# Performance work log

Measured on AMD Instinct MI355X. Metric: run time of the kernel, lower is better.

Reference implementation:

```python
import jax, jax.numpy as jnp
import numpy as np

EPS = 1e-5

def binarize(x):
    # sign with 0 -> -1
    return jnp.where(x <= 0, -1.0, 1.0).astype(x.dtype)

def conv2d(x, w, stride=1, padding=0, dilation=1):
    return jax.lax.conv_general_dilated(
        x, w, (stride, stride), [(padding, padding), (padding, padding)],
        rhs_dilation=(dilation, dilation),
        dimension_numbers=('NCHW', 'OIHW', 'NCHW'))

def bin_conv(x, w, stride=1, padding=0, dilation=1):
    return conv2d(binarize(x), binarize(w), stride, padding, dilation)

def bn(x, g, b, m, v):
    inv = g / jnp.sqrt(v + EPS)          # [C]
    return x * inv[None, :, None, None] + (b - m * inv)[None, :, None, None]

def prelu(x, a):
    return jnp.where(x >= 0, x, a * x)   # a is scalar (nn.PReLU default)

def setup_inputs() -> dict:
    key = jax.random.key(0)
    ks = jax.random.split(key, 16)
    B, C, H, W = 8, 128, 128, 256
    Ci = C // 4  # proj_ratio = 4
    def bn_params(k, c):
        k1, k2, k3, k4 = jax.random.split(k, 4)
        return (jax.random.uniform(k1, (c,), jnp.float32, 0.5, 1.5),
                jax.random.normal(k2, (c,), jnp.float32) * 0.1,
                jax.random.normal(k3, (c,), jnp.float32) * 0.1,
                jax.random.uniform(k4, (c,), jnp.float32, 0.5, 1.5))
    g1, b1, m1, v1 = bn_params(ks[1], Ci)
    g2, b2, m2, v2 = bn_params(ks[3], Ci)
    g3, b3, m3, v3 = bn_params(ks[5], C)
    return {
        'x': jax.random.normal(ks[0], (B, C, H, W), jnp.float32),
        'w1': jax.random.normal(ks[6], (Ci, C, 1, 1), jnp.float32) * 0.1,
        'g1': g1, 'b1': b1, 'm1': m1, 'v1': v1,
        'a1': jnp.float32(0.25),
        'w2': jax.random.normal(ks[7], (Ci, Ci, 3, 3), jnp.float32) * 0.1,
        'g2': g2, 'b2': b2, 'm2': m2, 'v2': v2,
        'a2': jnp.float32(0.25),
        'w3': jax.random.normal(ks[8], (C, Ci, 1, 1), jnp.float32) * 0.1,
        'g3': g3, 'b3': b3, 'm3': m3, 'v3': v3,
        'a3': jnp.float32(0.25),
        'a_out': jnp.float32(0.25),
    }

def reference(x, w1, g1, b1, m1, v1, a1,
              w2, g2, b2, m2, v2, a2,
              w3, g3, b3, m3, v3, a3, a_out):
    identity = x
    h = prelu(bn(bin_conv(x, w1), g1, b1, m1, v1), a1)          # 1x1 proj
    h = prelu(bn(bin_conv(h, w2, padding=1), g2, b2, m2, v2), a2)  # 3x3
    h = prelu(bn(bin_conv(h, w3), g3, b3, m3, v3), a3)          # 1x1 expand
    return prelu(h + identity, a_out)
```

## Files before the change

### kernel.cpp

```cpp
#include <hip/hip_runtime.h>
#include <stdint.h>
#include <math.h>


#define EPS 1e-5f
constexpr int B = 8, C = 128, Ci = 32, H = 128, W = 256;
constexpr int HW = H * W;
constexpr int P  = B * HW;

constexpr int WS_S1 = 1024;
constexpr int WS_S2 = 1024 + P;

__global__ __launch_bounds__(256) void prep_kernel(
    const float* __restrict__ w1,
    const float* __restrict__ g1, const float* __restrict__ b1,
    const float* __restrict__ m1, const float* __restrict__ v1,
    const float* __restrict__ w2,
    const float* __restrict__ g2, const float* __restrict__ b2,
    const float* __restrict__ m2, const float* __restrict__ v2,
    const float* __restrict__ w3,
    const float* __restrict__ g3, const float* __restrict__ b3,
    const float* __restrict__ m3, const float* __restrict__ v3,
    uint32_t* __restrict__ ws)
{
    int t = threadIdx.x;
    float* wsf = (float*)ws;

    if (t < 128) {
        int ci = t >> 2, wd = t & 3;
        const float* src = w1 + ci * C + wd * 32;
        uint32_t m = 0;
        #pragma unroll
        for (int j = 0; j < 32; ++j) m |= (src[j] > 0.f ? 1u : 0u) << j;
        ws[t] = m;
    }
    for (int idx = t; idx < 288; idx += 256) {
        int ci = idx / 9, tap = idx % 9;
        uint32_t m = 0;
        for (int cj = 0; cj < 32; ++cj)
            m |= (w2[(ci * Ci + cj) * 9 + tap] > 0.f ? 1u : 0u) << cj;
        ws[128 + idx] = m;
    }
    if (t < 128) {
        const float* src = w3 + t * Ci;
        uint32_t m = 0;
        #pragma unroll
        for (int j = 0; j < 32; ++j) m |= (src[j] > 0.f ? 1u : 0u) << j;
        ws[416 + t] = m;
    }
    if (t < 32) {
        float inv1 = g1[t] / sqrtf(v1[t] + EPS);
        wsf[544 + t] = m1[t] - b1[t] / inv1;
        float inv2 = g2[t] / sqrtf(v2[t] + EPS);
        wsf[576 + t] = m2[t] - b2[t] / inv2;
    }
    if (t < 128) {
        float i3 = g3[t] / sqrtf(v3[t] + EPS);
        wsf[608 + t] = i3;
        wsf[736 + t] = b3[t] - m3[t] * i3;
    }
}

__global__ __launch_bounds__(256) void k1_kernel(
    const float* __restrict__ x, const uint32_t* __restrict__ ws,
    uint32_t* __restrict__ s1)
{
    __shared__ uint32_t w1p[128];
    __shared__ float T1[32];
    int t = threadIdx.x;
    if (t < 128) w1p[t] = ws[t];
    if (t < 32)  T1[t] = ((const float*)ws)[544 + t];
    __syncthreads();

    int p0  = (blockIdx.x * 256 + t) * 4;
    int b   = p0 >> 15;
    int rem = p0 & (HW - 1);
    const float4* xb = (const float4*)(x + (size_t)b * C * HW) + (rem >> 2);
    constexpr int CS = HW / 4;

    uint32_t m[4][4];
    #pragma unroll
    for (int wd = 0; wd < 4; ++wd) {
        uint32_t m0 = 0, m1 = 0, m2 = 0, m3 = 0;
        #pragma unroll
        for (int j = 0; j < 32; ++j) {
            float4 v = xb[(size_t)(wd * 32 + j) * CS];
            m0 |= (v.x > 0.f ? 1u : 0u) << j;
            m1 |= (v.y > 0.f ? 1u : 0u) << j;
            m2 |= (v.z > 0.f ? 1u : 0u) << j;
            m3 |= (v.w > 0.f ? 1u : 0u) << j;
        }
        m[0][wd] = m0; m[1][wd] = m1; m[2][wd] = m2; m[3][wd] = m3;
    }

    uint32_t o0 = 0, o1 = 0, o2 = 0, o3 = 0;
    #pragma unroll
    for (int ci = 0; ci < 32; ++ci) {
        uint32_t wa = w1p[ci * 4 + 0], wb = w1p[ci * 4 + 1];
        uint32_t wc = w1p[ci * 4 + 2], wd = w1p[ci * 4 + 3];
        float T = T1[ci];
        int n0 = __popc(m[0][0] ^ wa) + __popc(m[0][1] ^ wb) + __popc(m[0][2] ^ wc) + __popc(m[0][3] ^ wd);
        int n1 = __popc(m[1][0] ^ wa) + __popc(m[1][1] ^ wb) + __popc(m[1][2] ^ wc) + __popc(m[1][3] ^ wd);
        int n2 = __popc(m[2][0] ^ wa) + __popc(m[2][1] ^ wb) + __popc(m[2][2] ^ wc) + __popc(m[2][3] ^ wd);
        int n3 = __popc(m[3][0] ^ wa) + __popc(m[3][1] ^ wb) + __popc(m[3][2] ^ wc) + __popc(m[3][3] ^ wd);
        o0 |= ((float)(128 - 2 * n0) > T ? 1u : 0u) << ci;
        o1 |= ((float)(128 - 2 * n1) > T ? 1u : 0u) << ci;
        o2 |= ((float)(128 - 2 * n2) > T ? 1u : 0u) << ci;
        o3 |= ((float)(128 - 2 * n3) > T ? 1u : 0u) << ci;
    }
    *(uint4*)(s1 + p0) = make_uint4(o0, o1, o2, o3);
}

__global__ __launch_bounds__(256) void k2_kernel(
    const uint32_t* __restrict__ s1, const uint32_t* __restrict__ ws,
    uint32_t* __restrict__ s2)
{
    __shared__ uint32_t w2p[288];
    __shared__ float T2[32];
    int t = threadIdx.x;
    for (int i = t; i < 288; i += 256) w2p[i] = ws[128 + i];
    if (t < 32) T2[t] = ((const float*)ws)[576 + t];
    __syncthreads();

    int p   = blockIdx.x * 256 + t;
    int b   = p >> 15;
    int rem = p & (HW - 1);
    int h   = rem >> 8;
    int w   = rem & 255;

    uint32_t n[9];
    uint32_t vmask = 0;
    int nv = 0;
    #pragma unroll
    for (int dy = -1; dy <= 1; ++dy) {
        #pragma unroll
        for (int dx = -1; dx <= 1; ++dx) {
            int tap = (dy + 1) * 3 + (dx + 1);
            int hh = h + dy, wv = w + dx;
            bool ok = (hh >= 0) & (hh < H) & (wv >= 0) & (wv < W);
            uint32_t val = 0;
            if (ok) val = s1[b * HW + hh * W + wv];
            n[tap] = val;
            vmask |= ok ? (1u << tap) : 0u;
            nv += ok ? 1 : 0;
        }
    }

    uint32_t out = 0;
    #pragma unroll
    for (int ci = 0; ci < 32; ++ci) {
        int neq = 0;
        #pragma unroll
        for (int tap = 0; tap < 9; ++tap) {
            int pc = __popc(n[tap] ^ w2p[ci * 9 + tap]);
            neq += ((vmask >> tap) & 1u) ? pc : 0;
        }
        float y2 = (float)(32 * nv - 2 * neq);
        out |= (y2 > T2[ci] ? 1u : 0u) << ci;
    }
    s2[p] = out;
}

__global__ __launch_bounds__(256) void k3_kernel(
    const float* __restrict__ x, const uint32_t* __restrict__ s2,
    const uint32_t* __restrict__ ws,
    const float* __restrict__ a3p, const float* __restrict__ aoutp,
    float* __restrict__ out)
{
    __shared__ uint32_t w3p[128];
    __shared__ float inv3[128], c3[128];
    int t = threadIdx.x;
    if (t < 128) {
        w3p[t]  = ws[416 + t];
        inv3[t] = ((const float*)ws)[608 + t];
        c3[t]   = ((const float*)ws)[736 + t];
    }
    __syncthreads();

    float a3 = a3p[0], aout = aoutp[0];
    int p   = blockIdx.x * 256 + t;
    int b   = p >> 15;
    int rem = p & (HW - 1);
    size_t base = (size_t)b * C * HW + rem;
    uint32_t sw = s2[p];

    #pragma unroll 8
    for (int c = 0; c < C; ++c) {
        int y3 = 32 - 2 * __popc(sw ^ w3p[c]);
        float hv = fmaf((float)y3, inv3[c], c3[c]);
        hv = hv < 0.f ? a3 * hv : hv;
        float o = hv + x[base + (size_t)c * HW];
        o = o < 0.f ? aout * o : o;
        out[base + (size_t)c * HW] = o;
    }
}

extern "C" void kernel_launch(void* const* d_in, const int* in_sizes, int n_in,
                              void* d_out, int out_size, void* d_ws, size_t ws_size,
                              hipStream_t stream)
{
    const float* x  = (const float*)d_in[0];
    const float* w1 = (const float*)d_in[1];
    const float* g1 = (const float*)d_in[2];
    const float* b1 = (const float*)d_in[3];
    const float* m1 = (const float*)d_in[4];
    const float* v1 = (const float*)d_in[5];
    const float* w2 = (const float*)d_in[7];
    const float* g2 = (const float*)d_in[8];
    const float* b2 = (const float*)d_in[9];
    const float* m2 = (const float*)d_in[10];
    const float* v2 = (const float*)d_in[11];
    const float* w3 = (const float*)d_in[13];
    const float* g3 = (const float*)d_in[14];
    const float* b3 = (const float*)d_in[15];
    const float* m3 = (const float*)d_in[16];
    const float* v3 = (const float*)d_in[17];
    const float* a3 = (const float*)d_in[18];
    const float* ao = (const float*)d_in[19];

    uint32_t* ws = (uint32_t*)d_ws;
    uint32_t* s1 = ws + WS_S1;
    uint32_t* s2 = ws + WS_S2;
    float* out = (float*)d_out;

    hipLaunchKernelGGL(prep_kernel, dim3(1), dim3(256), 0, stream,
                       w1, g1, b1, m1, v1, w2, g2, b2, m2, v2, w3, g3, b3, m3, v3, ws);
    hipLaunchKernelGGL(k1_kernel, dim3(P / 1024), dim3(256), 0, stream, x, ws, s1);
    hipLaunchKernelGGL(k2_kernel, dim3(P / 256), dim3(256), 0, stream, s1, ws, s2);
    hipLaunchKernelGGL(k3_kernel, dim3(P / 256), dim3(256), 0, stream, x, s2, ws, a3, ao, out);
}
```

Before: 310.7 us.

## Fuse 3x3 binary conv with expand stage, four pixels per thread

Merges the 3x3 binary convolution kernel into the final expand/residual kernel so the intermediate packed bitmask never goes to global memory. Each thread now processes four adjacent pixels, reusing a 3x6 neighbourhood of loaded words across them. This removes one launch and the s2 round trip but lowers thread count and raises register pressure in the memory-bound final loop.

Result: slower. 334.5 us (+7.6%).

```diff
diff --git a/kernel.cpp b/kernel.cpp
--- a/kernel.cpp
+++ b/kernel.cpp
@@ -9,7 +9,6 @@
 constexpr int P  = B * HW;
 
 constexpr int WS_S1 = 1024;
-constexpr int WS_S2 = 1024 + P;
 
 __global__ __launch_bounds__(256) void prep_kernel(
     const float* __restrict__ w1,
@@ -111,65 +110,19 @@
     *(uint4*)(s1 + p0) = make_uint4(o0, o1, o2, o3);
 }
 
-__global__ __launch_bounds__(256) void k2_kernel(
-    const uint32_t* __restrict__ s1, const uint32_t* __restrict__ ws,
-    uint32_t* __restrict__ s2)
+__global__ __launch_bounds__(256) void k23_kernel(
+    const float* __restrict__ x, const uint32_t* __restrict__ s1,
+    const uint32_t* __restrict__ ws,
+    const float* __restrict__ a3p, const float* __restrict__ aoutp,
+    float* __restrict__ out)
 {
     __shared__ uint32_t w2p[288];
     __shared__ float T2[32];
+    __shared__ uint32_t w3p[128];
+    __shared__ float inv3[128], c3[128];
     int t = threadIdx.x;
     for (int i = t; i < 288; i += 256) w2p[i] = ws[128 + i];
     if (t < 32) T2[t] = ((const float*)ws)[576 + t];
-    __syncthreads();
-
-    int p   = blockIdx.x * 256 + t;
-    int b   = p >> 15;
-    int rem = p & (HW - 1);
-    int h   = rem >> 8;
-    int w   = rem & 255;
-
-    uint32_t n[9];
-    uint32_t vmask = 0;
-    int nv = 0;
-    #pragma unroll
-    for (int dy = -1; dy <= 1; ++dy) {
-        #pragma unroll
-        for (int dx = -1; dx <= 1; ++dx) {
-            int tap = (dy + 1) * 3 + (dx + 1);
-            int hh = h + dy, wv = w + dx;
-            bool ok = (hh >= 0) & (hh < H) & (wv >= 0) & (wv < W);
-            uint32_t val = 0;
-            if (ok) val = s1[b * HW + hh * W + wv];
-            n[tap] = val;
-            vmask |= ok ? (1u << tap) : 0u;
-            nv += ok ? 1 : 0;
-        }
-    }
-
-    uint32_t out = 0;
-    #pragma unroll
-    for (int ci = 0; ci < 32; ++ci) {
-        int neq = 0;
-        #pragma unroll
-        for (int tap = 0; tap < 9; ++tap) {
-            int pc = __popc(n[tap] ^ w2p[ci * 9 + tap]);
-            neq += ((vmask >> tap) & 1u) ? pc : 0;
-        }
-        float y2 = (float)(32 * nv - 2 * neq);
-        out |= (y2 > T2[ci] ? 1u : 0u) << ci;
-    }
-    s2[p] = out;
-}
-
-__global__ __launch_bounds__(256) void k3_kernel(
-    const float* __restrict__ x, const uint32_t* __restrict__ s2,
-    const uint32_t* __restrict__ ws,
-    const float* __restrict__ a3p, const float* __restrict__ aoutp,
-    float* __restrict__ out)
-{
-    __shared__ uint32_t w3p[128];
-    __shared__ float inv3[128], c3[128];
-    int t = threadIdx.x;
     if (t < 128) {
         w3p[t]  = ws[416 + t];
         inv3[t] = ((const float*)ws)[608 + t];
@@ -177,21 +130,92 @@
     }
     __syncthreads();
 
+    int p0  = (blockIdx.x * 256 + t) * 4;
+    int b   = p0 >> 15;
+    int rem = p0 & (HW - 1);
+    int h   = rem >> 8;
+    int w0  = rem & 255;
+
+    const uint32_t* sb = s1 + b * HW;
+    uint32_t rowv[3][6];
+    uint32_t rokm = 0, colok = 0;
+    #pragma unroll
+    for (int i = 0; i < 6; ++i) {
+        int col = w0 - 1 + i;
+        if (col >= 0 && col < W) colok |= 1u << i;
+    }
+    #pragma unroll
+    for (int r = 0; r < 3; ++r) {
+        int hh = h - 1 + r;
+        bool rok = (hh >= 0) && (hh < H);
+        if (rok) rokm |= 1u << r;
+        #pragma unroll
+        for (int i = 0; i < 6; ++i) {
+            int col = w0 - 1 + i;
+            bool ok = rok && ((colok >> i) & 1u);
+            uint32_t val = 0;
+            if (ok) val = sb[hh * W + col];
+            rowv[r][i] = val;
+        }
+    }
+
+    uint32_t vm[4]; int nv[4];
+    #pragma unroll
+    for (int k = 0; k < 4; ++k) {
+        uint32_t v = 0;
+        #pragma unroll
+        for (int r = 0; r < 3; ++r) {
+            #pragma unroll
+            for (int dx = 0; dx < 3; ++dx) {
+                bool ok = ((rokm >> r) & 1u) && ((colok >> (k + dx)) & 1u);
+                v |= ok ? (1u << (r * 3 + dx)) : 0u;
+            }
+        }
+        vm[k] = v;
+        nv[k] = __popc(v);
+    }
+
+    uint32_t s2w[4] = {0, 0, 0, 0};
+    #pragma unroll
+    for (int ci = 0; ci < 32; ++ci) {
+        uint32_t wt[9];
+        #pragma unroll
+        for (int tap = 0; tap < 9; ++tap) wt[tap] = w2p[ci * 9 + tap];
+        float T = T2[ci];
+        #pragma unroll
+        for (int k = 0; k < 4; ++k) {
+            int neq = 0;
+            #pragma unroll
+            for (int r = 0; r < 3; ++r) {
+                #pragma unroll
+                for (int dx = 0; dx < 3; ++dx) {
+                    int tap = r * 3 + dx;
+                    int pc = __popc(rowv[r][k + dx] ^ wt[tap]);
+                    neq += ((vm[k] >> tap) & 1u) ? pc : 0;
+                }
+            }
+            float y2 = (float)(32 * nv[k] - 2 * neq);
+            s2w[k] |= (y2 > T ? 1u : 0u) << ci;
+        }
+    }
+
     float a3 = a3p[0], aout = aoutp[0];
-    int p   = blockIdx.x * 256 + t;
-    int b   = p >> 15;
-    int rem = p & (HW - 1);
     size_t base = (size_t)b * C * HW + rem;
-    uint32_t sw = s2[p];
-
-    #pragma unroll 8
+
+    #pragma unroll 4
     for (int c = 0; c < C; ++c) {
-        int y3 = 32 - 2 * __popc(sw ^ w3p[c]);
-        float hv = fmaf((float)y3, inv3[c], c3[c]);
-        hv = hv < 0.f ? a3 * hv : hv;
-        float o = hv + x[base + (size_t)c * HW];
-        o = o < 0.f ? aout * o : o;
-        out[base + (size_t)c * HW] = o;
+        uint32_t wc = w3p[c];
+        float iv = inv3[c], cc = c3[c];
+        size_t cb = base + (size_t)c * HW;
+        #pragma unroll
+        for (int k = 0; k < 4; ++k) {
+            int y3 = 32 - 2 * __popc(s2w[k] ^ wc);
+            float hv = fmaf((float)y3, iv, cc);
+            hv = hv < 0.f ? a3 * hv : hv;
+            float o = hv + x[cb + k];
+            o = o < 0.f ? aout * o : o;
+            out[cb + k] = o;
+        }
     }
 }
 
@@ -220,12 +244,11 @@
 
     uint32_t* ws = (uint32_t*)d_ws;
     uint32_t* s1 = ws + WS_S1;
-    uint32_t* s2 = ws + WS_S2;
     float* out = (float*)d_out;
 
     hipLaunchKernelGGL(prep_kernel, dim3(1), dim3(256), 0, stream,
                        w1, g1, b1, m1, v1, w2, g2, b2, m2, v2, w3, g3, b3, m3, v3, ws);
     hipLaunchKernelGGL(k1_kernel, dim3(P / 1024), dim3(256), 0, stream, x, ws, s1);
-    hipLaunchKernelGGL(k2_kernel, dim3(P / 256), dim3(256), 0, stream, s1, ws, s2);
-    hipLaunchKernelGGL(k3_kernel, dim3(P / 256), dim3(256), 0, stream, x, s2, ws, a3, ao, out);
-}
+    hipLaunchKernelGGL(k23_kernel, dim3(P / 1024), dim3(256), 0, stream,
+                       x, s1, ws, a3, ao, out);
+}
```
